# Kernel tuning notes

Hardware: AMD Instinct MI355X
Metric: run time of the kernel (lower is better)

The kernel has to match this reference:

```python
import jax, jax.numpy as jnp
import numpy as np

N_IN, N_OUT, K, G = 128, 256, 3, 3  # G = grid intervals (setup hard-codes 3)
KNOT_LO, KNOT_HI = -1.0, 1.0


def make_grid(n, k, G, lo=KNOT_LO, hi=KNOT_HI):
    # Augmented knot vector: G+1 knots extended by k on each side -> G+2k+1 points
    h = (hi - lo) / G
    g = jnp.arange(-k, G + k + 1, dtype=jnp.float32) * h + lo
    return jnp.tile(g[None, :], (n, 1))  # (n, G+2k+1)


def get_spline_basis(x, grid, k):
    # Cox-de Boor recursion. x: (batch, n); grid: (n, G+2k+1)
    g = grid[None, :, :]          # (1, n, G+2k+1)
    xx = x[:, :, None]            # (batch, n, 1)
    # order-0 (indicator) basis: (batch, n, G+2k)
    basis = ((xx >= g[..., :-1]) & (xx < g[..., 1:])).astype(x.dtype)
    for kk in range(1, k + 1):
        left = (xx - g[..., : -(kk + 1)]) / (g[..., kk:-1] - g[..., : -(kk + 1)]) * basis[..., :-1]
        right = (g[..., kk + 1 :] - xx) / (g[..., kk + 1 :] - g[..., 1:-kk]) * basis[..., 1:]
        basis = left + right
    return basis  # (batch, n, G+k)


def setup_inputs() -> dict:
    key = jax.random.key(0)
    k1, k2 = jax.random.split(key)
    batch = 512
    n = N_IN * N_OUT
    x = jax.random.normal(k1, (batch, N_IN), dtype=jnp.float32)
    grid = make_grid(n, K, G)                                        # state (non-trainable)
    c_basis = 0.1 * jax.random.normal(k2, (n, G + K), dtype=jnp.float32)
    c_spl = jnp.ones((n,), dtype=jnp.float32)
    c_res = jnp.ones((n,), dtype=jnp.float32)
    return {"x": x, "grid": grid, "c_basis": c_basis, "c_spl": c_spl, "c_res": c_res}


def reference(x, grid, c_basis, c_spl, c_res):
    batch = x.shape[0]
    # Broadcast each input node to every output edge, out-major ordering:
    # einsum('ij,k->ikj', x, ones(n_out)).reshape(batch, n_in*n_out)
    x_ext = jnp.broadcast_to(x[:, None, :], (batch, N_OUT, N_IN)).reshape(batch, N_OUT * N_IN)
    # residual branch: swish, transposed to (n, batch)
    res = jax.nn.swish(x_ext).T
    # spline branch: (batch, n, G+K) basis combined with per-edge coeffs -> (n, batch)
    Bi = get_spline_basis(x_ext, grid, K)
    spl = jnp.einsum('ij,bij->ib', c_basis, Bi)
    y = c_spl[:, None] * spl + c_res[:, None] * res            # (n, batch)
    y = y.reshape(N_OUT, N_IN, batch).sum(axis=1) / N_IN       # (n_out, batch)
    return y.T                                                 # (batch, n_out)
```

## Files before the change

### kernel.cpp

```cpp
#include <hip/hip_runtime.h>
#include <hip/hip_bf16.h>
#include <math.h>


typedef short short8 __attribute__((ext_vector_type(8)));
typedef float f32x4 __attribute__((ext_vector_type(4)));

#define KDIM 896
#define KPAD 904

static __device__ inline unsigned short bf16_bits(float f) {
    union { __hip_bfloat16 h; unsigned short u; } cvt;
    cvt.h = __float2bfloat16(f);
    return cvt.u;
}

__global__ __launch_bounds__(128) void kan_fused(
    const float* __restrict__ x,
    const float* __restrict__ grid,
    const float* __restrict__ c_basis,
    const float* __restrict__ c_spl,
    const float* __restrict__ c_res,
    float* __restrict__ out)
{
    extern __shared__ __align__(16) unsigned short smem[];
    unsigned short* Fs = smem;
    unsigned short* Ws = smem + 16 * KPAD;

    const int bt  = blockIdx.x >> 3;
    const int ot  = blockIdx.x & 7;
    const int tid = threadIdx.x;

    float t[10];
#pragma unroll
    for (int m = 0; m < 10; ++m) t[m] = grid[m];
    const float ih1 = 1.0f / (t[1] - t[0]);
    const float ih2 = 1.0f / (t[2] - t[0]);
    const float ih3 = 1.0f / (t[3] - t[0]);

#pragma unroll 4
    for (int p = 0; p < 16; ++p) {
        const float xv = x[(bt * 16 + p) * 128 + tid];

        float b0[9];
#pragma unroll
        for (int s = 0; s < 9; ++s)
            b0[s] = (xv >= t[s] && xv < t[s + 1]) ? 1.0f : 0.0f;
        float b1[8];
#pragma unroll
        for (int s = 0; s < 8; ++s)
            b1[s] = (xv - t[s]) * ih1 * b0[s] + (t[s + 2] - xv) * ih1 * b0[s + 1];
        float b2[7];
#pragma unroll
        for (int s = 0; s < 7; ++s)
            b2[s] = (xv - t[s]) * ih2 * b1[s] + (t[s + 3] - xv) * ih2 * b1[s + 1];
        float b3[6];
#pragma unroll
        for (int s = 0; s < 6; ++s)
            b3[s] = (xv - t[s]) * ih3 * b2[s] + (t[s + 4] - xv) * ih3 * b2[s + 1];

        const float sw = xv / (1.0f + expf(-xv));

        unsigned short* dst = Fs + p * KPAD + tid * 7;
#pragma unroll
        for (int s = 0; s < 6; ++s) dst[s] = bf16_bits(b3[s]);
        dst[6] = bf16_bits(sw);
    }

#pragma unroll 4
    for (int p = 0; p < 32; ++p) {
        const int j = (ot * 32 + p) * 128 + tid;
        const float spl = c_spl[j];
        unsigned short* dst = Ws + p * KPAD + tid * 7;
#pragma unroll
        for (int s = 0; s < 6; ++s) dst[s] = bf16_bits(spl * c_basis[j * 6 + s]);
        dst[6] = bf16_bits(c_res[j]);
    }

    __syncthreads();

    const int lane = tid & 63;
    const int w    = tid >> 6;
    const int r    = lane & 15;
    const int q    = lane >> 4;

    const unsigned short* fa = Fs + r * KPAD + q * 8;
    const unsigned short* wb = Ws + (w * 16 + r) * KPAD + q * 8;

    f32x4 acc0 = {0.f, 0.f, 0.f, 0.f};
    f32x4 acc1 = {0.f, 0.f, 0.f, 0.f};

#pragma unroll
    for (int k0 = 0; k0 < KDIM; k0 += 64) {
        short8 a0 = *(const short8*)(fa + k0);
        short8 a1 = *(const short8*)(fa + k0 + 32);
        short8 b0 = *(const short8*)(wb + k0);
        short8 b1 = *(const short8*)(wb + k0 + 32);
        acc0 = __builtin_amdgcn_mfma_f32_16x16x32_bf16(a0, b0, acc0, 0, 0, 0);
        acc1 = __builtin_amdgcn_mfma_f32_16x16x32_bf16(a1, b1, acc1, 0, 0, 0);
    }

    const float scale = 1.0f / 128.0f;
    const int orow0 = bt * 16 + q * 4;
    const int ocol  = ot * 32 + w * 16 + r;
#pragma unroll
    for (int e = 0; e < 4; ++e)
        out[(orow0 + e) * 256 + ocol] = (acc0[e] + acc1[e]) * scale;
}

extern "C" void kernel_launch(void* const* d_in, const int* in_sizes, int n_in,
                              void* d_out, int out_size, void* d_ws, size_t ws_size,
                              hipStream_t stream) {
    const float* x       = (const float*)d_in[0];
    const float* grid    = (const float*)d_in[1];
    const float* c_basis = (const float*)d_in[2];
    const float* c_spl   = (const float*)d_in[3];
    const float* c_res   = (const float*)d_in[4];
    float* out = (float*)d_out;

    const size_t smem_bytes = (16 + 32) * KPAD * sizeof(unsigned short);
    kan_fused<<<256, 128, smem_bytes, stream>>>(x, grid, c_basis, c_spl, c_res, out);
}
```

Before: 72.40 us.

## Use 512-thread blocks with split-K MFMA reduction and closed-form cubic B-spline

```diff
diff --git a/kernel.cpp b/kernel.cpp
--- a/kernel.cpp
+++ b/kernel.cpp
@@ -15,7 +15,7 @@
     return cvt.u;
 }
 
-__global__ __launch_bounds__(128) void kan_fused(
+__global__ __launch_bounds__(512) void kan_fused(
     const float* __restrict__ x,
     const float* __restrict__ grid,
     const float* __restrict__ c_basis,
@@ -23,89 +23,113 @@
     const float* __restrict__ c_res,
     float* __restrict__ out)
 {
-    extern __shared__ __align__(16) unsigned short smem[];
-    unsigned short* Fs = smem;
-    unsigned short* Ws = smem + 16 * KPAD;
+    extern __shared__ __align__(16) unsigned char smem[];
+    unsigned short* Fs = (unsigned short*)smem;
+    unsigned short* Ws = Fs + 16 * KPAD;
+    float*          Red = (float*)(smem + 48 * KPAD * 2);
 
     const int bt  = blockIdx.x >> 3;
     const int ot  = blockIdx.x & 7;
     const int tid = threadIdx.x;
+    const int col = tid & 127;
+    const int grp = tid >> 7;
 
-    float t[10];
+    const float t0 = grid[0];
+    const float ih = 1.0f / (grid[1] - grid[0]);
+
 #pragma unroll
-    for (int m = 0; m < 10; ++m) t[m] = grid[m];
-    const float ih1 = 1.0f / (t[1] - t[0]);
-    const float ih2 = 1.0f / (t[2] - t[0]);
-    const float ih3 = 1.0f / (t[3] - t[0]);
+    for (int pp = 0; pp < 4; ++pp) {
+        const int p  = grp * 4 + pp;
+        const float xv = x[(bt * 16 + p) * 128 + col];
 
-#pragma unroll 4
-    for (int p = 0; p < 16; ++p) {
-        const float xv = x[(bt * 16 + p) * 128 + tid];
+        const float xr = (xv - t0) * ih;
+        const float sf = floorf(xr);
+        const int   s  = (int)sf;
+        const float u  = xr - sf;
+        const float um = 1.0f - u;
+        const float uu = u * u;
+        const float p0 = (1.0f / 6.0f) * uu * u;
+        const float p3 = (1.0f / 6.0f) * um * um * um;
+        const float p1 = (1.0f / 6.0f) * (((-3.0f * u + 3.0f) * u + 3.0f) * u + 1.0f);
+        const float p2 = (1.0f / 6.0f) * ((3.0f * u - 6.0f) * uu + 4.0f);
 
-        float b0[9];
+        unsigned short* dst = Fs + p * KPAD + col * 7;
 #pragma unroll
-        for (int s = 0; s < 9; ++s)
-            b0[s] = (xv >= t[s] && xv < t[s + 1]) ? 1.0f : 0.0f;
-        float b1[8];
-#pragma unroll
-        for (int s = 0; s < 8; ++s)
-            b1[s] = (xv - t[s]) * ih1 * b0[s] + (t[s + 2] - xv) * ih1 * b0[s + 1];
-        float b2[7];
-#pragma unroll
-        for (int s = 0; s < 7; ++s)
-            b2[s] = (xv - t[s]) * ih2 * b1[s] + (t[s + 3] - xv) * ih2 * b1[s + 1];
-        float b3[6];
-#pragma unroll
-        for (int s = 0; s < 6; ++s)
-            b3[s] = (xv - t[s]) * ih3 * b2[s] + (t[s + 4] - xv) * ih3 * b2[s + 1];
-
-        const float sw = xv / (1.0f + expf(-xv));
-
-        unsigned short* dst = Fs + p * KPAD + tid * 7;
-#pragma unroll
-        for (int s = 0; s < 6; ++s) dst[s] = bf16_bits(b3[s]);
+        for (int t = 0; t < 6; ++t) {
+            const int d = s - t;
+            const float v = (d == 0) ? p0 : (d == 1) ? p1 : (d == 2) ? p2
+                          : (d == 3) ? p3 : 0.0f;
+            dst[t] = bf16_bits(v);
+        }
+        const float sw = xv / (1.0f + __expf(-xv));
         dst[6] = bf16_bits(sw);
     }
 
-#pragma unroll 4
-    for (int p = 0; p < 32; ++p) {
-        const int j = (ot * 32 + p) * 128 + tid;
+#pragma unroll
+    for (int pp = 0; pp < 8; ++pp) {
+        const int p = grp * 8 + pp;
+        const int j = (ot * 32 + p) * 128 + col;
         const float spl = c_spl[j];
-        unsigned short* dst = Ws + p * KPAD + tid * 7;
+        unsigned short* dst = Ws + p * KPAD + col * 7;
 #pragma unroll
-        for (int s = 0; s < 6; ++s) dst[s] = bf16_bits(spl * c_basis[j * 6 + s]);
+        for (int t = 0; t < 6; ++t) dst[t] = bf16_bits(spl * c_basis[j * 6 + t]);
         dst[6] = bf16_bits(c_res[j]);
     }
 
     __syncthreads();
 
+    const int w    = tid >> 6;
     const int lane = tid & 63;
-    const int w    = tid >> 6;
     const int r    = lane & 15;
     const int q    = lane >> 4;
+    const int ho   = w & 1;
+    const int kq   = w >> 1;
 
-    const unsigned short* fa = Fs + r * KPAD + q * 8;
-    const unsigned short* wb = Ws + (w * 16 + r) * KPAD + q * 8;
+    const unsigned short* fa = Fs + r * KPAD + q * 8 + kq * 224;
+    const unsigned short* wb = Ws + (ho * 16 + r) * KPAD + q * 8 + kq * 224;
 
     f32x4 acc0 = {0.f, 0.f, 0.f, 0.f};
     f32x4 acc1 = {0.f, 0.f, 0.f, 0.f};
-
 #pragma unroll
-    for (int k0 = 0; k0 < KDIM; k0 += 64) {
+    for (int k0 = 0; k0 < 192; k0 += 64) {
         short8 a0 = *(const short8*)(fa + k0);
+        short8 b0 = *(const short8*)(wb + k0);
         short8 a1 = *(const short8*)(fa + k0 + 32);
-        short8 b0 = *(const short8*)(wb + k0);
         short8 b1 = *(const short8*)(wb + k0 + 32);
         acc0 = __builtin_amdgcn_mfma_f32_16x16x32_bf16(a0, b0, acc0, 0, 0, 0);
         acc1 = __builtin_amdgcn_mfma_f32_16x16x32_bf16(a1, b1, acc1, 0, 0, 0);
     }
+    {
+        short8 a0 = *(const short8*)(fa + 192);
+        short8 b0 = *(const short8*)(wb + 192);
+        acc0 = __builtin_amdgcn_mfma_f32_16x16x32_bf16(a0, b0, acc0, 0, 0, 0);
+    }
+    f32x4 acc;
+#pragma unroll
+    for (int e = 0; e < 4; ++e) acc[e] = acc0[e] + acc1[e];
 
-    const float scale = 1.0f / 128.0f;
-    const int orow0 = bt * 16 + q * 4;
-    const int ocol  = ot * 32 + w * 16 + r;
+    if (kq > 0) {
+        float* dst = Red + (((kq - 1) * 2 + ho) * 64 + lane) * 4;
+        *(f32x4*)dst = acc;
+    }
+    __syncthreads();
+
+    if (kq == 0) {
+        const float* r0 = Red + ((0 * 2 + ho) * 64 + lane) * 4;
+        const float* r1 = Red + ((1 * 2 + ho) * 64 + lane) * 4;
+        const float* r2 = Red + ((2 * 2 + ho) * 64 + lane) * 4;
+        const f32x4 v0 = *(const f32x4*)r0;
+        const f32x4 v1 = *(const f32x4*)r1;
+        const f32x4 v2 = *(const f32x4*)r2;
+
+        const float scale = 1.0f / 128.0f;
+        const int orow0 = bt * 16 + q * 4;
+        const int ocol  = ot * 32 + ho * 16 + r;
 #pragma unroll
-    for (int e = 0; e < 4; ++e)
-        out[(orow0 + e) * 256 + ocol] = (acc0[e] + acc1[e]) * scale;
+        for (int e = 0; e < 4; ++e)
+            out[(orow0 + e) * 256 + ocol] =
+                (acc[e] + v0[e] + v1[e] + v2[e]) * scale;
+    }
 }
 
 extern "C" void kernel_launch(void* const* d_in, const int* in_sizes, int n_in,
@@ -118,6 +142,6 @@
     const float* c_res   = (const float*)d_in[4];
     float* out = (float*)d_out;
 
-    const size_t smem_bytes = (16 + 32) * KPAD * sizeof(unsigned short);
-    kan_fused<<<256, 128, smem_bytes, stream>>>(x, grid, c_basis, c_spl, c_res, out);
+    const size_t smem_bytes = 48 * KPAD * 2 + 6 * 256 * 4;
+    kan_fused<<<256, 512, smem_bytes, stream>>>(x, grid, c_basis, c_spl, c_res, out);
 }
```

After: 68.55 us. -5.3%, faster.
